# Kernel tuning notes

Hardware: AMD Instinct MI355X
Metric: run time of the kernel (lower is better)

Reference implementation:

```python
import jax, jax.numpy as jnp
import numpy as np

DEPTH = 3  # args.depth (chemprop default)


def setup_inputs() -> dict:
    key = jax.random.key(0)
    ks = jax.random.split(key, 10)
    n_atoms, n_bonds, max_nb, n_mols = 100000, 200000, 6, 4000
    H, AF, BF = 300, 133, 147  # hidden_size, atom_fdim, bond_fdim

    f_atoms = jax.random.normal(ks[0], (n_atoms, AF), jnp.float32)
    f_bonds = jax.random.normal(ks[1], (n_bonds, BF), jnp.float32)
    a2b = jax.random.randint(ks[2], (n_atoms, max_nb), 0, n_bonds)      # incoming bonds per atom
    b2a = jax.random.randint(ks[3], (n_bonds,), 0, n_atoms)             # source atom per bond
    b2revb = jax.random.randint(ks[4], (n_bonds,), 0, n_bonds)          # reverse bond index
    atom_mol = jnp.sort(jax.random.randint(ks[5], (n_atoms,), 0, n_mols))  # contiguous mol segments (a_scope)

    # Learned params (W_i, W_h bias-free per args.bias=False; W_o has bias)
    W_i = jax.random.normal(ks[6], (BF, H), jnp.float32) * (1.0 / np.sqrt(BF))
    W_h = jax.random.normal(ks[7], (H, H), jnp.float32) * (1.0 / np.sqrt(H))
    W_o = jax.random.normal(ks[8], (AF + H, H), jnp.float32) * (1.0 / np.sqrt(AF + H))
    b_o = jax.random.normal(ks[9], (H,), jnp.float32) * 0.01

    return dict(f_atoms=f_atoms, f_bonds=f_bonds, W_i=W_i, W_h=W_h, W_o=W_o, b_o=b_o,
                a2b=a2b, b2a=b2a, b2revb=b2revb, atom_mol=atom_mol, n_mols=n_mols)


def reference(f_atoms, f_bonds, W_i, W_h, W_o, b_o, a2b, b2a, b2revb, atom_mol, n_mols):
    # Bond-message D-MPNN (atom_messages=False), ReLU activation, dropout=0 (eval)
    inp = f_bonds @ W_i                       # [n_bonds, H]
    message = jax.nn.relu(inp)
    for _ in range(DEPTH - 1):
        nei_a_message = message[a2b]          # [n_atoms, max_nb, H] gather
        a_message = nei_a_message.sum(axis=1) # [n_atoms, H]
        message = a_message[b2a] - message[b2revb]  # [n_bonds, H]
        message = jax.nn.relu(inp + message @ W_h)
    # Atom readout
    a_message = message[a2b].sum(axis=1)      # [n_atoms, H]
    a_input = jnp.concatenate([f_atoms, a_message], axis=1)
    atom_hiddens = jax.nn.relu(a_input @ W_o + b_o)  # [n_atoms, H]
    # Per-molecule mean aggregation (a_scope loop -> segment ops)
    sums = jax.ops.segment_sum(atom_hiddens, atom_mol, num_segments=n_mols)
    counts = jax.ops.segment_sum(jnp.ones((atom_hiddens.shape[0],), atom_hiddens.dtype),
                                 atom_mol, num_segments=n_mols)
    return sums / jnp.maximum(counts, 1.0)[:, None]  # empty mols -> zero vector
```

## Files before the change

### kernel.cpp

```cpp
#include <hip/hip_runtime.h>
#include <hip/hip_bf16.h>
#include <stdint.h>


#define H_DIM 300
#define HP 320
#define AF_DIM 133
#define BF_DIM 147
#define MAXNB 6

typedef __hip_bfloat16 bf16;
typedef __attribute__((ext_vector_type(8))) short short8;
typedef __attribute__((ext_vector_type(4))) float f32x4;

__device__ __forceinline__ float b2f_raw(unsigned short u) {
    union { unsigned int i; float f; } v; v.i = ((unsigned int)u) << 16; return v.f;
}
__device__ __forceinline__ unsigned short f2b_raw(float f) {
    union { float f; unsigned int i; } v; v.f = f;
    unsigned int x = v.i;
    x += 0x7fffu + ((x >> 16) & 1u);
    return (unsigned short)(x >> 16);
}

__global__ __launch_bounds__(256) void prep_wt(
    const float* __restrict__ s1, int r1,
    const float* __restrict__ s2, int r2,
    unsigned short* __restrict__ Wt, int nkt)
{
    const int Ktot = nkt * 32;
    const int idx = blockIdx.x * 256 + threadIdx.x;
    if (idx >= 320 * Ktot) return;
    const int n = idx % 320;
    const int k = idx / 320;
    float v = 0.f;
    if (n < H_DIM) {
        if (k < 320) { if (k < r1) v = s1[k * H_DIM + n]; }
        else { const int kk = k - 320; if (kk < r2) v = s2[kk * H_DIM + n]; }
    }
    Wt[n * Ktot + k] = f2b_raw(v);
}

template <int MODE>
__global__ __launch_bounds__(256) void mfma_gemm(
    const bf16* __restrict__ Ab,
    const bf16* __restrict__ Ab2,
    const float* __restrict__ Afp,
    const int* __restrict__ idx1,
    const int* __restrict__ idx2,
    const unsigned short* __restrict__ Wt,
    const float* __restrict__ bias,
    bf16* __restrict__ out,
    int M)
{
    constexpr int NKT  = (MODE == 1) ? 5 : 15;
    constexpr int KTOT = NKT * 32;
    constexpr int FPW  = (MODE == 3) ? AF_DIM : BF_DIM;

    __shared__ char As[2][64 * 64];
    __shared__ char Cs[16 * 640];

    const int t    = threadIdx.x;
    const int m0   = blockIdx.x * 64;
    const int wave = t >> 6;
    const int lane = t & 63;
    const int l16  = lane & 15;
    const int quad = lane >> 4;
    const int swz  = ((quad ^ (l16 & 3)) << 4);

    const int am  = t >> 2;
    const int c   = t & 3;
    const int gm  = m0 + am;
    const bool mok = (gm < M);
    const int aoff = am * 64 + ((c ^ (am & 3)) << 4);

    long rowA = 0, rowB = 0;
    if (MODE == 2 && mok) { rowA = idx1[gm]; rowB = idx2[gm]; }

    auto load_a = [&](int kt) -> uint4 {
        uint4 aval = {0u, 0u, 0u, 0u};
        if (!mok) return aval;
        if (MODE == 1) {
            const int k = kt * 32 + c * 8;
            unsigned short* rp = (unsigned short*)&aval;
#pragma unroll
            for (int j = 0; j < 8; ++j) {
                const int kk = k + j;
                rp[j] = (kk < BF_DIM) ? f2b_raw(Afp[(long)gm * BF_DIM + kk]) : 0;
            }
        } else if (kt < 10) {
            const int k = kt * 32 + c * 8;
            if (MODE == 2) {
                const uint4 a4 = *(const uint4*)((const char*)Ab  + (rowA * HP + k) * 2);
                const uint4 b4 = *(const uint4*)((const char*)Ab2 + (rowB * HP + k) * 2);
                const unsigned short* ap = (const unsigned short*)&a4;
                const unsigned short* bp = (const unsigned short*)&b4;
                unsigned short* rp = (unsigned short*)&aval;
#pragma unroll
                for (int j = 0; j < 8; ++j)
                    rp[j] = f2b_raw(b2f_raw(ap[j]) - b2f_raw(bp[j]));
            } else {
                aval = *(const uint4*)((const char*)Ab + ((long)gm * HP + k) * 2);
            }
        } else {
            const int k2 = (kt - 10) * 32 + c * 8;
            unsigned short* rp = (unsigned short*)&aval;
#pragma unroll
            for (int j = 0; j < 8; ++j) {
                const int kk = k2 + j;
                rp[j] = (kk < FPW) ? f2b_raw(Afp[(long)gm * FPW + kk]) : 0;
            }
        }
        return aval;
    };

    auto load_b = [&](int kt, short8* bfr) {
        const int kbase = kt * 32 + quad * 8;
#pragma unroll
        for (int nt = 0; nt < 5; ++nt) {
            const int nn = wave * 80 + nt * 16 + l16;
            bfr[nt] = *(const short8*)(Wt + (long)nn * KTOT + kbase);
        }
    };

    f32x4 acc[4][5];
#pragma unroll
    for (int i = 0; i < 4; ++i)
#pragma unroll
        for (int j = 0; j < 5; ++j) acc[i][j] = (f32x4){0.f, 0.f, 0.f, 0.f};

    uint4 aval = load_a(0);
    *(uint4*)(As[0] + aoff) = aval;
    short8 bfr[5];
    load_b(0, bfr);

    for (int kt = 0; kt < NKT; ++kt) {
        short8 bfr_n[5];
        if (kt + 1 < NKT) {
            aval = load_a(kt + 1);
            load_b(kt + 1, bfr_n);
        }
        __syncthreads();
        short8 afr[4];
#pragma unroll
        for (int mt = 0; mt < 4; ++mt)
            afr[mt] = *(const short8*)(As[kt & 1] + mt * 1024 + l16 * 64 + swz);
#pragma unroll
        for (int nt = 0; nt < 5; ++nt)
#pragma unroll
            for (int mt = 0; mt < 4; ++mt)
                acc[mt][nt] = __builtin_amdgcn_mfma_f32_16x16x32_bf16(
                    afr[mt], bfr[nt], acc[mt][nt], 0, 0, 0);
        if (kt + 1 < NKT) {
            *(uint4*)(As[(kt + 1) & 1] + aoff) = aval;
#pragma unroll
            for (int nt = 0; nt < 5; ++nt) bfr[nt] = bfr_n[nt];
        }
    }

    for (int mt = 0; mt < 4; ++mt) {
        __syncthreads();
#pragma unroll
        for (int nt = 0; nt < 5; ++nt) {
            const int col = wave * 80 + nt * 16 + l16;
            float bv = 0.f;
            if (MODE == 3) bv = (col < H_DIM) ? bias[col] : 0.f;
#pragma unroll
            for (int r = 0; r < 4; ++r) {
                const float v = fmaxf(acc[mt][nt][r] + bv, 0.f);
                ((unsigned short*)Cs)[(quad * 4 + r) * HP + col] = f2b_raw(v);
            }
        }
        __syncthreads();
        const int gr0 = m0 + mt * 16;
#pragma unroll
        for (int i = 0; i < 3; ++i) {
            const int idx = i * 256 + t;
            if (idx < 640) {
                const int row = idx / 40;
                if (gr0 + row < M)
                    *(uint4*)((char*)out + (long)(gr0 + row) * 640 + (idx - row * 40) * 16)
                        = *(const uint4*)(Cs + idx * 16);
            }
        }
    }
}

__global__ __launch_bounds__(256) void gather_sum_kernel(
    const bf16* __restrict__ msg, const int* __restrict__ a2b,
    bf16* __restrict__ amsg, int n_atoms)
{
    const int idx = blockIdx.x * 256 + threadIdx.x;
    if (idx >= n_atoms * (HP / 8)) return;
    const int a = idx / (HP / 8);
    const int cc = idx - a * (HP / 8);
    float s[8] = {0.f, 0.f, 0.f, 0.f, 0.f, 0.f, 0.f, 0.f};
    const int base = a * MAXNB;
#pragma unroll
    for (int j = 0; j < MAXNB; ++j) {
        const long b = a2b[base + j];
        const uint4 u = *(const uint4*)((const char*)msg + (b * HP + cc * 8) * 2);
        const unsigned short* up = (const unsigned short*)&u;
#pragma unroll
        for (int e = 0; e < 8; ++e) s[e] += b2f_raw(up[e]);
    }
    uint4 r;
    unsigned short* rp = (unsigned short*)&r;
#pragma unroll
    for (int e = 0; e < 8; ++e) rp[e] = f2b_raw(s[e]);
    *(uint4*)((char*)amsg + ((long)a * HP + cc * 8) * 2) = r;
}

__global__ __launch_bounds__(256) void seg_mean_kernel(
    const bf16* __restrict__ hidden, const int* __restrict__ atom_mol,
    float* __restrict__ out, int n_atoms)
{
    const int m = blockIdx.x;
    __shared__ int s_lo, s_hi;
    if (threadIdx.x == 0) {
        int lo = 0, hi = n_atoms;
        while (lo < hi) { int mid = (lo + hi) >> 1; if (atom_mol[mid] < m) lo = mid + 1; else hi = mid; }
        s_lo = lo;
        int lo2 = lo; hi = n_atoms;
        while (lo2 < hi) { int mid = (lo2 + hi) >> 1; if (atom_mol[mid] < m + 1) lo2 = mid + 1; else hi = mid; }
        s_hi = lo2;
    }
    __syncthreads();
    const int lo = s_lo, hi = s_hi;
    const float inv = 1.0f / (float)max(hi - lo, 1);
    for (int cpass = 0; cpass < 2; ++cpass) {
        const int c = cpass * 256 + threadIdx.x;
        if (c >= H_DIM) break;
        float s = 0.f;
        for (int a = lo; a < hi; ++a)
            s += b2f_raw(((const unsigned short*)hidden)[(long)a * HP + c]);
        out[(long)m * H_DIM + c] = s * inv;
    }
}

extern "C" void kernel_launch(void* const* d_in, const int* in_sizes, int n_in,
                              void* d_out, int out_size, void* d_ws, size_t ws_size,
                              hipStream_t stream)
{
    const float* f_atoms = (const float*)d_in[0];
    const float* f_bonds = (const float*)d_in[1];
    const float* W_i     = (const float*)d_in[2];
    const float* W_h     = (const float*)d_in[3];
    const float* W_o     = (const float*)d_in[4];
    const float* b_o     = (const float*)d_in[5];
    const int*  a2b      = (const int*)d_in[6];
    const int*  b2a      = (const int*)d_in[7];
    const int*  b2revb   = (const int*)d_in[8];
    const int*  atom_mol = (const int*)d_in[9];

    const int n_atoms = in_sizes[0] / AF_DIM;
    const int n_bonds = in_sizes[1] / BF_DIM;
    const int n_mols  = out_size / H_DIM;

    char* ws = (char*)d_ws;
    size_t off = 0;
    auto alloc = [&](size_t bytes) {
        size_t o = off; off += (bytes + 255) & ~(size_t)255; return o;
    };
    bf16* msgA = (bf16*)(ws + alloc((size_t)n_bonds * HP * 2));
    bf16* msgB = (bf16*)(ws + alloc((size_t)n_bonds * HP * 2));
    bf16* amsg = (bf16*)(ws + alloc((size_t)n_atoms * HP * 2));
    unsigned short* Wt1 = (unsigned short*)(ws + alloc(320 * 160 * 2));
    unsigned short* Wt2 = (unsigned short*)(ws + alloc(320 * 480 * 2));
    unsigned short* Wt3 = (unsigned short*)(ws + alloc(320 * 480 * 2));
    bf16* hidden = msgB;

    const dim3 blk(256);

    prep_wt<<<(320 * 160 + 255) / 256, blk, 0, stream>>>(W_i, BF_DIM, nullptr, 0, Wt1, 5);
    prep_wt<<<(320 * 480 + 255) / 256, blk, 0, stream>>>(W_h, H_DIM, W_i, BF_DIM, Wt2, 15);
    prep_wt<<<(320 * 480 + 255) / 256, blk, 0, stream>>>(W_o + (size_t)AF_DIM * H_DIM, H_DIM,
                                                         W_o, AF_DIM, Wt3, 15);

    const int gB = (n_bonds + 63) / 64;
    const int gA = (n_atoms + 63) / 64;
    const int gG = (n_atoms * (HP / 8) + 255) / 256;

    mfma_gemm<1><<<gB, blk, 0, stream>>>(nullptr, nullptr, f_bonds, nullptr, nullptr,
                                         Wt1, nullptr, msgA, n_bonds);
    gather_sum_kernel<<<gG, blk, 0, stream>>>(msgA, a2b, amsg, n_atoms);
    mfma_gemm<2><<<gB, blk, 0, stream>>>(amsg, msgA, f_bonds, b2a, b2revb,
                                         Wt2, nullptr, msgB, n_bonds);
    gather_sum_kernel<<<gG, blk, 0, stream>>>(msgB, a2b, amsg, n_atoms);
    mfma_gemm<2><<<gB, blk, 0, stream>>>(amsg, msgB, f_bonds, b2a, b2revb,
                                         Wt2, nullptr, msgA, n_bonds);
    gather_sum_kernel<<<gG, blk, 0, stream>>>(msgA, a2b, amsg, n_atoms);
    mfma_gemm<3><<<gA, blk, 0, stream>>>(amsg, nullptr, f_atoms, nullptr, nullptr,
                                         Wt3, b_o, hidden, n_atoms);
    seg_mean_kernel<<<n_mols, blk, 0, stream>>>(hidden, atom_mol, (float*)d_out, n_atoms);
}
```

Baseline: 928.6 us.

## Deepen A-operand prefetch to two stages and split load from convert

Restructures the GEMM main loop so global loads for the A tile are issued two k-steps ahead and their bf16 conversion is deferred, and B fragments are fetched one step ahead unconditionally. Bounds checks are replaced by clamping row and column indices, and 32-bit offsets replace 64-bit address math. A raw s_barrier with an explicit lgkmcnt wait and a sched_barrier stand in for __syncthreads to control instruction placement. This aims to hide gather and global memory latency behind MFMA work, at the cost of more registers, which may reduce occupancy, and redundant clamped loads for out-of-range rows.

```diff
diff --git a/kernel.cpp b/kernel.cpp
--- a/kernel.cpp
+++ b/kernel.cpp
@@ -68,50 +68,52 @@
     const int quad = lane >> 4;
     const int swz  = ((quad ^ (l16 & 3)) << 4);
 
-    const int am  = t >> 2;
-    const int c   = t & 3;
-    const int gm  = m0 + am;
-    const bool mok = (gm < M);
+    const int am   = t >> 2;
+    const int c    = t & 3;
+    const int gm   = min(m0 + am, M - 1);
     const int aoff = am * 64 + ((c ^ (am & 3)) << 4);
 
-    long rowA = 0, rowB = 0;
-    if (MODE == 2 && mok) { rowA = idx1[gm]; rowB = idx2[gm]; }
-
-    auto load_a = [&](int kt) -> uint4 {
-        uint4 aval = {0u, 0u, 0u, 0u};
-        if (!mok) return aval;
-        if (MODE == 1) {
-            const int k = kt * 32 + c * 8;
-            unsigned short* rp = (unsigned short*)&aval;
+    int offA = 0, offB = 0;
+    if (MODE == 2) { offA = idx1[gm] * 640; offB = idx2[gm] * 640; }
+    if (MODE == 3) { offA = gm * 640; }
+    const char* AbC  = (const char*)Ab;
+    const char* Ab2C = (const char*)Ab2;
+
+    auto issue_a = [&](int kt, uint4& x, uint4& y) {
+        if (MODE != 1 && kt < 10) {
+            const int koff = kt * 64 + c * 16;
+            x = *(const uint4*)(AbC + (unsigned)(offA + koff));
+            if (MODE == 2) y = *(const uint4*)(Ab2C + (unsigned)(offB + koff));
+        } else {
+            const int kb = (MODE == 1 ? kt * 32 : (kt - 10) * 32) + c * 8;
+            float* xp = (float*)&x;
+            float* yp = (float*)&y;
 #pragma unroll
             for (int j = 0; j < 8; ++j) {
-                const int kk = k + j;
-                rp[j] = (kk < BF_DIM) ? f2b_raw(Afp[(long)gm * BF_DIM + kk]) : 0;
+                const int kk = min(kb + j, FPW - 1);
+                const float v = Afp[gm * FPW + kk];
+                if (j < 4) xp[j] = v; else yp[j - 4] = v;
             }
-        } else if (kt < 10) {
-            const int k = kt * 32 + c * 8;
-            if (MODE == 2) {
-                const uint4 a4 = *(const uint4*)((const char*)Ab  + (rowA * HP + k) * 2);
-                const uint4 b4 = *(const uint4*)((const char*)Ab2 + (rowB * HP + k) * 2);
-                const unsigned short* ap = (const unsigned short*)&a4;
-                const unsigned short* bp = (const unsigned short*)&b4;
-                unsigned short* rp = (unsigned short*)&aval;
-#pragma unroll
-                for (int j = 0; j < 8; ++j)
-                    rp[j] = f2b_raw(b2f_raw(ap[j]) - b2f_raw(bp[j]));
-            } else {
-                aval = *(const uint4*)((const char*)Ab + ((long)gm * HP + k) * 2);
-            }
+        }
+    };
+    auto conv_a = [&](int kt, const uint4& x, const uint4& y) -> uint4 {
+        uint4 r;
+        unsigned short* rp = (unsigned short*)&r;
+        if (MODE == 1 || kt >= 10) {
+            const float* xp = (const float*)&x;
+            const float* yp = (const float*)&y;
+#pragma unroll
+            for (int j = 0; j < 8; ++j) rp[j] = f2b_raw(j < 4 ? xp[j] : yp[j - 4]);
+        } else if (MODE == 2) {
+            const unsigned short* ap = (const unsigned short*)&x;
+            const unsigned short* bp = (const unsigned short*)&y;
+#pragma unroll
+            for (int j = 0; j < 8; ++j)
+                rp[j] = f2b_raw(b2f_raw(ap[j]) - b2f_raw(bp[j]));
         } else {
-            const int k2 = (kt - 10) * 32 + c * 8;
-            unsigned short* rp = (unsigned short*)&aval;
-#pragma unroll
-            for (int j = 0; j < 8; ++j) {
-                const int kk = k2 + j;
-                rp[j] = (kk < FPW) ? f2b_raw(Afp[(long)gm * FPW + kk]) : 0;
-            }
-        }
-        return aval;
+            r = x;
+        }
+        return r;
     };
 
     auto load_b = [&](int kt, short8* bfr) {
@@ -129,33 +131,33 @@
 #pragma unroll
         for (int j = 0; j < 5; ++j) acc[i][j] = (f32x4){0.f, 0.f, 0.f, 0.f};
 
-    uint4 aval = load_a(0);
-    *(uint4*)(As[0] + aoff) = aval;
-    short8 bfr[5];
+    uint4 x0, y0, x1, y1;
+    issue_a(0, x0, y0);
+    *(uint4*)(As[0] + aoff) = conv_a(0, x0, y0);
+    short8 bfr[5], bfr_n[5];
     load_b(0, bfr);
+    issue_a(1, x0, y0);
 
     for (int kt = 0; kt < NKT; ++kt) {
-        short8 bfr_n[5];
-        if (kt + 1 < NKT) {
-            aval = load_a(kt + 1);
-            load_b(kt + 1, bfr_n);
-        }
-        __syncthreads();
-        short8 afr[4];
-#pragma unroll
-        for (int mt = 0; mt < 4; ++mt)
-            afr[mt] = *(const short8*)(As[kt & 1] + mt * 1024 + l16 * 64 + swz);
-#pragma unroll
-        for (int nt = 0; nt < 5; ++nt)
-#pragma unroll
-            for (int mt = 0; mt < 4; ++mt)
+        const int ktn  = (kt + 1 < NKT) ? kt + 1 : NKT - 1;
+        const int ktn2 = (kt + 2 < NKT) ? kt + 2 : NKT - 1;
+        load_b(ktn, bfr_n);
+        issue_a(ktn2, x1, y1);
+        asm volatile("s_waitcnt lgkmcnt(0)" ::: "memory");
+        __builtin_amdgcn_s_barrier();
+#pragma unroll
+        for (int mt = 0; mt < 4; ++mt) {
+            const short8 afr = *(const short8*)(As[kt & 1] + mt * 1024 + l16 * 64 + swz);
+#pragma unroll
+            for (int nt = 0; nt < 5; ++nt)
                 acc[mt][nt] = __builtin_amdgcn_mfma_f32_16x16x32_bf16(
-                    afr[mt], bfr[nt], acc[mt][nt], 0, 0, 0);
-        if (kt + 1 < NKT) {
-            *(uint4*)(As[(kt + 1) & 1] + aoff) = aval;
-#pragma unroll
-            for (int nt = 0; nt < 5; ++nt) bfr[nt] = bfr_n[nt];
-        }
+                    afr, bfr[nt], acc[mt][nt], 0, 0, 0);
+        }
+        __builtin_amdgcn_sched_barrier(0);
+        *(uint4*)(As[(kt + 1) & 1] + aoff) = conv_a(ktn, x0, y0);
+        x0 = x1; y0 = y1;
+#pragma unroll
+        for (int nt = 0; nt < 5; ++nt) bfr[nt] = bfr_n[nt];
     }
 
     for (int mt = 0; mt < 4; ++mt) {
```

Measured after the change: 1.075 ms. 1.16x slower.

## Reassociate W_h GEMM before gather: multiply messages first, then gather-combine

Applied to the files above, without the earlier changes.

Uses linearity to compute message@W_h per bond first, then gathers and sums the projected rows and subtracts the reverse bond's projected row. This lets the GEMM run on contiguous rows with K=320 instead of doing an indexed gather-subtract inside a K=480 GEMM. It also stores the input projection once and adds it in a separate elementwise combine kernel that applies the ReLU. The cost is an extra full-size bond buffer, an extra combine kernel per iteration, and bf16 rounding of intermediate products that differs from the original order.

```diff
diff --git a/kernel.cpp b/kernel.cpp
--- a/kernel.cpp
+++ b/kernel.cpp
@@ -41,21 +41,19 @@
     Wt[n * Ktot + k] = f2b_raw(v);
 }
 
-template <int MODE>
+template <int MODE, bool RELU_A>
 __global__ __launch_bounds__(256) void mfma_gemm(
     const bf16* __restrict__ Ab,
-    const bf16* __restrict__ Ab2,
     const float* __restrict__ Afp,
-    const int* __restrict__ idx1,
-    const int* __restrict__ idx2,
     const unsigned short* __restrict__ Wt,
     const float* __restrict__ bias,
     bf16* __restrict__ out,
     int M)
 {
-    constexpr int NKT  = (MODE == 1) ? 5 : 15;
+    constexpr int NKT  = (MODE == 1) ? 5 : (MODE == 4 ? 10 : 15);
     constexpr int KTOT = NKT * 32;
     constexpr int FPW  = (MODE == 3) ? AF_DIM : BF_DIM;
+    constexpr bool RELU_OUT = (MODE == 3);
 
     __shared__ char As[2][64 * 64];
     __shared__ char Cs[16 * 640];
@@ -74,9 +72,6 @@
     const bool mok = (gm < M);
     const int aoff = am * 64 + ((c ^ (am & 3)) << 4);
 
-    long rowA = 0, rowB = 0;
-    if (MODE == 2 && mok) { rowA = idx1[gm]; rowB = idx2[gm]; }
-
     auto load_a = [&](int kt) -> uint4 {
         uint4 aval = {0u, 0u, 0u, 0u};
         if (!mok) return aval;
@@ -88,19 +83,14 @@
                 const int kk = k + j;
                 rp[j] = (kk < BF_DIM) ? f2b_raw(Afp[(long)gm * BF_DIM + kk]) : 0;
             }
-        } else if (kt < 10) {
+        } else if (MODE == 4 || kt < 10) {
             const int k = kt * 32 + c * 8;
-            if (MODE == 2) {
-                const uint4 a4 = *(const uint4*)((const char*)Ab  + (rowA * HP + k) * 2);
-                const uint4 b4 = *(const uint4*)((const char*)Ab2 + (rowB * HP + k) * 2);
-                const unsigned short* ap = (const unsigned short*)&a4;
-                const unsigned short* bp = (const unsigned short*)&b4;
+            aval = *(const uint4*)((const char*)Ab + ((long)gm * HP + k) * 2);
+            if (RELU_A) {
                 unsigned short* rp = (unsigned short*)&aval;
 #pragma unroll
                 for (int j = 0; j < 8; ++j)
-                    rp[j] = f2b_raw(b2f_raw(ap[j]) - b2f_raw(bp[j]));
-            } else {
-                aval = *(const uint4*)((const char*)Ab + ((long)gm * HP + k) * 2);
+                    rp[j] = (rp[j] & 0x8000u) ? 0 : rp[j];
             }
         } else {
             const int k2 = (kt - 10) * 32 + c * 8;
@@ -167,7 +157,8 @@
             if (MODE == 3) bv = (col < H_DIM) ? bias[col] : 0.f;
 #pragma unroll
             for (int r = 0; r < 4; ++r) {
-                const float v = fmaxf(acc[mt][nt][r] + bv, 0.f);
+                float v = acc[mt][nt][r] + bv;
+                if (RELU_OUT) v = fmaxf(v, 0.f);
                 ((unsigned short*)Cs)[(quad * 4 + r) * HP + col] = f2b_raw(v);
             }
         }
@@ -209,6 +200,34 @@
 #pragma unroll
     for (int e = 0; e < 8; ++e) rp[e] = f2b_raw(s[e]);
     *(uint4*)((char*)amsg + ((long)a * HP + cc * 8) * 2) = r;
+}
+
+__global__ __launch_bounds__(256) void combine_kernel(
+    const bf16* __restrict__ inp, const bf16* __restrict__ Gh,
+    const bf16* __restrict__ Hm, const int* __restrict__ b2a,
+    const int* __restrict__ b2revb, bf16* __restrict__ outm, int n_bonds)
+{
+    const int idx = blockIdx.x * 256 + threadIdx.x;
+    if (idx >= n_bonds * (HP / 8)) return;
+    const int b = idx / (HP / 8);
+    const int cc = idx - b * (HP / 8);
+    const long co = (long)cc * 16;
+    const long ra = b2a[b];
+    const long rb = b2revb[b];
+    const uint4 vi = *(const uint4*)((const char*)inp + (long)b * 640 + co);
+    const uint4 vg = *(const uint4*)((const char*)Gh + ra * 640 + co);
+    const uint4 vh = *(const uint4*)((const char*)Hm + rb * 640 + co);
+    const unsigned short* ip = (const unsigned short*)&vi;
+    const unsigned short* gp = (const unsigned short*)&vg;
+    const unsigned short* hp = (const unsigned short*)&vh;
+    uint4 r;
+    unsigned short* rp = (unsigned short*)&r;
+#pragma unroll
+    for (int e = 0; e < 8; ++e) {
+        const float v = b2f_raw(ip[e]) + b2f_raw(gp[e]) - b2f_raw(hp[e]);
+        rp[e] = f2b_raw(fmaxf(v, 0.f));
+    }
+    *(uint4*)((char*)outm + (long)b * 640 + co) = r;
 }
 
 __global__ __launch_bounds__(256) void seg_mean_kernel(
@@ -262,35 +281,39 @@
     auto alloc = [&](size_t bytes) {
         size_t o = off; off += (bytes + 255) & ~(size_t)255; return o;
     };
-    bf16* msgA = (bf16*)(ws + alloc((size_t)n_bonds * HP * 2));
-    bf16* msgB = (bf16*)(ws + alloc((size_t)n_bonds * HP * 2));
+    bf16* inpB = (bf16*)(ws + alloc((size_t)n_bonds * HP * 2));
+    bf16* msgX = (bf16*)(ws + alloc((size_t)n_bonds * HP * 2));
+    bf16* HmB  = (bf16*)(ws + alloc((size_t)n_bonds * HP * 2));
     bf16* amsg = (bf16*)(ws + alloc((size_t)n_atoms * HP * 2));
     unsigned short* Wt1 = (unsigned short*)(ws + alloc(320 * 160 * 2));
-    unsigned short* Wt2 = (unsigned short*)(ws + alloc(320 * 480 * 2));
+    unsigned short* WtH = (unsigned short*)(ws + alloc(320 * 320 * 2));
     unsigned short* Wt3 = (unsigned short*)(ws + alloc(320 * 480 * 2));
-    bf16* hidden = msgB;
+    bf16* hidden = HmB;
 
     const dim3 blk(256);
 
     prep_wt<<<(320 * 160 + 255) / 256, blk, 0, stream>>>(W_i, BF_DIM, nullptr, 0, Wt1, 5);
-    prep_wt<<<(320 * 480 + 255) / 256, blk, 0, stream>>>(W_h, H_DIM, W_i, BF_DIM, Wt2, 15);
+    prep_wt<<<(320 * 320 + 255) / 256, blk, 0, stream>>>(W_h, H_DIM, nullptr, 0, WtH, 10);
     prep_wt<<<(320 * 480 + 255) / 256, blk, 0, stream>>>(W_o + (size_t)AF_DIM * H_DIM, H_DIM,
                                                          W_o, AF_DIM, Wt3, 15);
 
     const int gB = (n_bonds + 63) / 64;
     const int gA = (n_atoms + 63) / 64;
     const int gG = (n_atoms * (HP / 8) + 255) / 256;
-
-    mfma_gemm<1><<<gB, blk, 0, stream>>>(nullptr, nullptr, f_bonds, nullptr, nullptr,
-                                         Wt1, nullptr, msgA, n_bonds);
-    gather_sum_kernel<<<gG, blk, 0, stream>>>(msgA, a2b, amsg, n_atoms);
-    mfma_gemm<2><<<gB, blk, 0, stream>>>(amsg, msgA, f_bonds, b2a, b2revb,
-                                         Wt2, nullptr, msgB, n_bonds);
-    gather_sum_kernel<<<gG, blk, 0, stream>>>(msgB, a2b, amsg, n_atoms);
-    mfma_gemm<2><<<gB, blk, 0, stream>>>(amsg, msgB, f_bonds, b2a, b2revb,
-                                         Wt2, nullptr, msgA, n_bonds);
-    gather_sum_kernel<<<gG, blk, 0, stream>>>(msgA, a2b, amsg, n_atoms);
-    mfma_gemm<3><<<gA, blk, 0, stream>>>(amsg, nullptr, f_atoms, nullptr, nullptr,
-                                         Wt3, b_o, hidden, n_atoms);
+    const int gC = (n_bonds * (HP / 8) + 255) / 256;
+
+    mfma_gemm<1, false><<<gB, blk, 0, stream>>>(nullptr, f_bonds, Wt1, nullptr, inpB, n_bonds);
+
+    mfma_gemm<4, true><<<gB, blk, 0, stream>>>(inpB, nullptr, WtH, nullptr, HmB, n_bonds);
+    gather_sum_kernel<<<gG, blk, 0, stream>>>(HmB, a2b, amsg, n_atoms);
+    combine_kernel<<<gC, blk, 0, stream>>>(inpB, amsg, HmB, b2a, b2revb, msgX, n_bonds);
+
+    mfma_gemm<4, false><<<gB, blk, 0, stream>>>(msgX, nullptr, WtH, nullptr, HmB, n_bonds);
+    gather_sum_kernel<<<gG, blk, 0, stream>>>(HmB, a2b, amsg, n_atoms);
+    combine_kernel<<<gC, blk, 0, stream>>>(inpB, amsg, HmB, b2a, b2revb, msgX, n_bonds);
+
+    gather_sum_kernel<<<gG, blk, 0, stream>>>(msgX, a2b, amsg, n_atoms);
+    mfma_gemm<3, false><<<gA, blk, 0, stream>>>(amsg, f_atoms, Wt3, b_o, hidden, n_atoms);
+
     seg_mean_kernel<<<n_mols, blk, 0, stream>>>(hidden, atom_mol, (float*)d_out, n_atoms);
 }
```

New measurement: 960.6 us. 1.03x slower.
